# Kernel tuning notes

Hardware: AMD Instinct MI355X
Metric: run time of the kernel (lower is better)

Reference implementation:

```python
import jax
import jax.numpy as jnp
import numpy as np

KSIZE, STRIDE, RATE, FUSE_K, SCALE = 3, 1, 2, 3, 10.0
ESCAPE_NAN = 1e-4


def _same_pad(x, k, s):
    # replicates torch same_padding: asymmetric zero pad so out = ceil(H/s)
    H, W = x.shape[2], x.shape[3]
    oh, ow = -(-H // s), -(-W // s)
    ph = max(0, (oh - 1) * s + k - H)
    pw = max(0, (ow - 1) * s + k - W)
    return jnp.pad(x, ((0, 0), (0, 0), (ph // 2, ph - ph // 2), (pw // 2, pw - pw // 2)))


def _extract_patches(x, k, s):
    # torch extract_image_patches: -> [B, L, C, k, k] with L = out_h*out_w
    x = _same_pad(x, k, s)
    B, C, H, W = x.shape
    Ho, Wo = (H - k) // s + 1, (W - k) // s + 1
    slices = [x[:, :, i:i + Ho * s:s, j:j + Wo * s:s] for i in range(k) for j in range(k)]
    p = jnp.stack(slices, axis=2).reshape(B, C, k, k, Ho, Wo)
    return p.transpose(0, 4, 5, 1, 2, 3).reshape(B, Ho * Wo, C, k, k)


def _contextual_attention(f, b, mask):
    dn = ('NCHW', 'OIHW', 'NCHW')
    # raw background patches for the final deconv: k = 2*rate, stride = rate
    raw_pat = _extract_patches(b, 2 * RATE, RATE * STRIDE)  # [B, L, C, 4, 4]
    # nearest-neighbor 1/rate downsample (torch F.interpolate nearest, sf=0.5)
    f_ds = f[:, :, ::RATE, ::RATE]
    b_ds = b[:, :, ::RATE, ::RATE]
    m_ds = mask[:, :, ::RATE, ::RATE]
    B, C, Hf, Wf = f_ds.shape
    Hb, Wb = b_ds.shape[2], b_ds.shape[3]
    b_pat = _extract_patches(b_ds, KSIZE, STRIDE)  # [B, L, C, 3, 3], L = Hb*Wb
    m_pat = _extract_patches(m_ds, KSIZE, STRIDE)[0]  # [L, 1, 3, 3] (first sample only, as in torch)
    mm = (jnp.mean(m_pat, axis=(1, 2, 3)) == 0.0).astype(f.dtype)[None, :, None, None]  # [1, L, 1, 1]
    fuse_w = jnp.eye(FUSE_K, dtype=f.dtype).reshape(1, 1, FUSE_K, FUSE_K)

    def per_item(xi, wi, raw_wi):
        # xi: [C,Hf,Wf]; wi: [L,C,3,3]; raw_wi: [L,C,4,4]
        max_wi = jnp.sqrt(jnp.sum(wi * wi + ESCAPE_NAN, axis=(1, 2, 3), keepdims=True))
        wi_n = wi / max_wi
        # matching conv: scores [1, L, Hf, Wf]
        yi = jax.lax.conv_general_dilated(xi[None], wi_n, (1, 1), ((1, 1), (1, 1)), dimension_numbers=dn)
        # fuse: identity-diagonal 3x3 conv along (bg_idx, fg_idx) twice with transposes
        yi = yi.reshape(1, 1, Hb * Wb, Hf * Wf)
        yi = jax.lax.conv_general_dilated(yi, fuse_w, (1, 1), ((1, 1), (1, 1)), dimension_numbers=dn)
        yi = yi.reshape(Hb, Wb, Hf, Wf).transpose(1, 0, 3, 2).reshape(1, 1, Hb * Wb, Hf * Wf)
        yi = jax.lax.conv_general_dilated(yi, fuse_w, (1, 1), ((1, 1), (1, 1)), dimension_numbers=dn)
        yi = yi.reshape(Wb, Hb, Wf, Hf).transpose(1, 0, 3, 2).reshape(1, Hb * Wb, Hf, Wf)
        yi = yi * mm
        yi = jax.nn.softmax(yi * SCALE, axis=1) * mm
        # conv_transpose2d(yi, raw_wi[I=L,O=C], stride=rate, padding=1) / 4
        w2 = jnp.flip(raw_wi, (2, 3)).transpose(1, 0, 2, 3)  # [C, L, 4, 4]
        pad = 2 * RATE - 1 - 1  # k - 1 - torch_padding = 2
        out = jax.lax.conv_general_dilated(yi, w2, (1, 1), ((pad, pad), (pad, pad)),
                                           lhs_dilation=(RATE, RATE), dimension_numbers=dn) / 4.0
        return out[0]

    return jax.vmap(per_item)(f_ds, b_pat, raw_pat)  # [B, C, H, W]


def setup_inputs() -> dict:
    key = jax.random.key(0)
    k1, k2 = jax.random.split(key)
    B, C, H, W = 2, 128, 128, 128
    f = jax.random.normal(k1, (B, C, H, W), dtype=jnp.float32)
    b = jax.random.normal(k2, (B, C, H, W), dtype=jnp.float32)
    mask = jnp.zeros((B, 1, H, W), dtype=jnp.float32)
    return {"f": f, "b": b, "mask": mask}


def reference(f, b, mask):
    return _contextual_attention(f, b, mask)
```

## Files before the change

### kernel.cpp

```cpp
#include <hip/hip_runtime.h>
#include <math.h>

#define CDIM 128
#define HF   128
#define WF   128
#define NP   4096
#define NCHUNK 64

typedef __attribute__((ext_vector_type(8))) short short8;
typedef __attribute__((ext_vector_type(16))) float f16a;
typedef float __attribute__((ext_vector_type(4), aligned(16))) f4a16;
typedef float __attribute__((ext_vector_type(4), aligned(4)))  f4u;

__device__ inline ushort f2bf(float x) {
  union { float f; unsigned u; } v; v.f = x;
  unsigned r = v.u + 0x7fff + ((v.u >> 16) & 1);
  return (ushort)(r >> 16);
}
__device__ inline float bf2f(ushort h) {
  union { unsigned u; float f; } v; v.u = ((unsigned)h) << 16; return v.f;
}

__device__ inline void gl2lds16(const ushort* g, ushort* l) {
  __builtin_amdgcn_global_load_lds((const __attribute__((address_space(1))) void*)g,
                                   (__attribute__((address_space(3))) void*)l, 16, 0, 0);
}

__global__ __launch_bounds__(256) void k_prep(const float* __restrict__ f,
                                              const float* __restrict__ b,
                                              ushort* __restrict__ fcat,
                                              ushort* __restrict__ bcat,
                                              float* __restrict__ s2) {
  int idx = blockIdx.x * 256 + threadIdx.x;
  int c = idx & 127, pos = idx >> 7;
  int x = pos & 63, y = pos >> 6;
  int src = c * 16384 + y * 256 + x * 2;
  float fv = f[src], bv = b[src];
  ushort fh = f2bf(fv); ushort fl = f2bf(fv - bf2f(fh));
  ushort bh = f2bf(bv); ushort bl = f2bf(bv - bf2f(bh));
  size_t base = (size_t)pos * 384;
  fcat[base + c] = fh; fcat[base + 128 + c] = fl; fcat[base + 256 + c] = fh;
  bcat[base + c] = bh; bcat[base + 128 + c] = bh; bcat[base + 256 + c] = bl;
  float sq = bv * bv;
#pragma unroll
  for (int off = 32; off; off >>= 1) sq += __shfl_down(sq, off);
  __shared__ float wsum[4];
  if ((threadIdx.x & 63) == 0) wsum[threadIdx.x >> 6] = sq;
  __syncthreads();
  if (threadIdx.x == 0) s2[blockIdx.x * 2]     = wsum[0] + wsum[1];
  if (threadIdx.x == 1) s2[blockIdx.x * 2 + 1] = wsum[2] + wsum[3];
}

__global__ __launch_bounds__(256) void k_mmpnorm(const float* __restrict__ mask,
                                                 const float* __restrict__ s2,
                                                 float* __restrict__ mmp,
                                                 float* __restrict__ rnrm) {
  int bx = blockIdx.x, t = threadIdx.x;
  if (bx < 16) {
    int a = bx * 256 + t;
    int yb = a & 63, xb = a >> 6;
    float s = 0.f;
    for (int dy = -1; dy <= 1; ++dy)
      for (int dx = -1; dx <= 1; ++dx) {
        int y = yb + dy, x = xb + dx;
        if ((unsigned)y < 64u && (unsigned)x < 64u)
          s += mask[y * 256 + x * 2];
      }
    mmp[a] = (s == 0.0f) ? 1.0f : 0.0f;
  } else {
    int p = (bx - 16) * 256 + t;
    int xb = p & 63, yb = p >> 6;
    float s = 0.f;
    for (int dy = -1; dy <= 1; ++dy)
      for (int dx = -1; dx <= 1; ++dx) {
        int y = yb + dy, x = xb + dx;
        if ((unsigned)y < 64u && (unsigned)x < 64u) s += s2[y * 64 + x];
      }
    rnrm[p] = rsqrtf(s + 1152.0f * 1.0e-4f);
  }
}

__global__ __launch_bounds__(512) void k_mfma_gemm(const ushort* __restrict__ A,
                                                   const ushort* __restrict__ B,
                                                   float* __restrict__ Out,
                                                   int Kdim, int lda, int ldb, int ldo,
                                                   long osplit) {
  __shared__ ushort As[2][256 * 64];
  __shared__ ushort Bs[2][256 * 64];
  const int tid = threadIdx.x;
  const int wave = tid >> 6, lane = tid & 63;
  const int l32 = lane & 31, khalf = lane >> 5;

  unsigned nbx = gridDim.x, nby = gridDim.y;
  unsigned lid = blockIdx.x + nbx * (blockIdx.y + nby * blockIdx.z);
  unsigned cpx = (nbx * nby * gridDim.z) >> 3;
  unsigned swz = (lid & 7) * cpx + (lid >> 3);
  unsigned bx = swz % nbx;
  unsigned tmp = swz / nbx;
  unsigned by = tmp % nby, bz = tmp / nby;

  const int m0 = by * 256, n0 = bx * 256;
  const int wm = (wave >> 2) * 128, wn = (wave & 3) * 64;
  const int srow = lane >> 3;
  const int gperm = ((lane & 7) ^ srow) * 8;

  const int koff = bz * Kdim;
  A += koff; B += koff;
  Out += (size_t)bz * osplit;

  const ushort* Ag = A + (size_t)(m0 + wave * 8 + srow) * lda + gperm;
  const ushort* Bg = B + (size_t)(n0 + wave * 8 + srow) * ldb + gperm;
  ushort* AsW = &As[0][0] + (wave * 8) * 64;
  ushort* BsW = &Bs[0][0] + (wave * 8) * 64;

#define STG_A(sl, tt, q) gl2lds16(Ag + (size_t)((q) * 64) * lda + ((tt) << 6), \
                                  AsW + (sl) * 16384 + (q) * 4096)
#define STG_B(sl, tt, q) gl2lds16(Bg + (size_t)((q) * 64) * ldb + ((tt) << 6), \
                                  BsW + (sl) * 16384 + (q) * 4096)

  f16a acc[4][2];
#pragma unroll
  for (int u = 0; u < 4; ++u)
#pragma unroll
    for (int v = 0; v < 2; ++v)
#pragma unroll
      for (int r = 0; r < 16; ++r) acc[u][v][r] = 0.f;

  const int NT = Kdim >> 6;

#pragma unroll
  for (int q = 0; q < 4; ++q) { STG_A(0, 0, q); STG_B(0, 0, q); }
  if (NT > 1) {
#pragma unroll
    for (int q = 0; q < 4; ++q) { STG_A(1, 1, q); STG_B(1, 1, q); }
    asm volatile("s_waitcnt vmcnt(8)" ::: "memory");
  } else {
    asm volatile("s_waitcnt vmcnt(0)" ::: "memory");
  }
  __builtin_amdgcn_s_barrier();

  for (int t = 0; t < NT; ++t) {
    const int sl = t & 1;
    const ushort* Ar = &As[sl][0];
    const ushort* Br = &Bs[sl][0];
    short8 af[2][4], bf[2][2];

#define FRAG_READS(sidx) do { \
  _Pragma("unroll") for (int u = 0; u < 4; ++u) { \
    int am = wm + u * 32 + l32; \
    int ga = (((sidx) * 2 + khalf) ^ (am & 7)) * 8; \
    af[(sidx) & 1][u] = *reinterpret_cast<const short8*>(&Ar[am * 64 + ga]); } \
  _Pragma("unroll") for (int v = 0; v < 2; ++v) { \
    int bn = wn + v * 32 + l32; \
    int gb = (((sidx) * 2 + khalf) ^ (bn & 7)) * 8; \
    bf[(sidx) & 1][v] = *reinterpret_cast<const short8*>(&Br[bn * 64 + gb]); } \
} while (0)

    FRAG_READS(0);
#pragma unroll
    for (int s = 0; s < 4; ++s) {
      if (s == 1) FRAG_READS(2);
      if (s == 2) FRAG_READS(3);
      if (s == 0) FRAG_READS(1);
      if (s == 3) {
        asm volatile("s_waitcnt lgkmcnt(0)" ::: "memory");
        __builtin_amdgcn_sched_barrier(0);
        __builtin_amdgcn_s_barrier();
        __builtin_amdgcn_sched_barrier(0);
        if (t + 2 < NT) {
#pragma unroll
          for (int q = 0; q < 4; ++q) { STG_A(sl, t + 2, q); STG_B(sl, t + 2, q); }
        }
        __builtin_amdgcn_s_setprio(1);
      }
#pragma unroll
      for (int u = 0; u < 4; ++u)
#pragma unroll
        for (int v = 0; v < 2; ++v)
          acc[u][v] = __builtin_amdgcn_mfma_f32_32x32x16_bf16(af[s & 1][u], bf[s & 1][v],
                                                              acc[u][v], 0, 0, 0);
      if (s == 3) __builtin_amdgcn_s_setprio(0);
    }
    if (t + 1 < NT) {
      if (t + 2 < NT) asm volatile("s_waitcnt vmcnt(8)" ::: "memory");
      else            asm volatile("s_waitcnt vmcnt(0)" ::: "memory");
      __builtin_amdgcn_s_barrier();
    }
#undef FRAG_READS
  }

#pragma unroll
  for (int u = 0; u < 4; ++u)
#pragma unroll
    for (int v = 0; v < 2; ++v)
#pragma unroll
      for (int r = 0; r < 16; ++r) {
        int row = (r & 3) + 8 * (r >> 2) + 4 * khalf;
        Out[(size_t)(m0 + wm + u * 32 + row) * ldo + (n0 + wn + v * 32 + l32)] = acc[u][v][r];
      }
#undef STG_A
#undef STG_B
}

__global__ __launch_bounds__(256) void k_s0(const float* __restrict__ D,
                                            const float* __restrict__ rnrm,
                                            float* __restrict__ S0) {
  int p = ((blockIdx.x & 7) << 9) | (blockIdx.x >> 3);
  int yb = p >> 6, xb = p & 63;
  float rp = rnrm[p];
  int t = threadIdx.x;
#pragma unroll
  for (int it = 0; it < 4; ++it) {
    int q = (it * 256 + t) << 2;
    int qy = q >> 6, qx = q & 63;
    f4a16 acc = (f4a16){0.f, 0.f, 0.f, 0.f};
#pragma unroll
    for (int dy = -1; dy <= 1; ++dy) {
      if ((unsigned)(yb + dy) >= 64u) continue;
      if ((unsigned)(qy + dy) >= 64u) continue;
#pragma unroll
      for (int dx = -1; dx <= 1; ++dx) {
        if ((unsigned)(xb + dx) >= 64u) continue;
        int delta = dy * 64 + dx;
        const float* base = D + (size_t)(p + delta) * 4096;
        f4u v;
        if (dx == -1 && qx == 0) {
          f4u r = *(const f4u*)(base + q + delta + 1);
          v = (f4u){0.f, r.x, r.y, r.z};
        } else {
          v = *(const f4u*)(base + q + delta);
          if (dx == 1 && qx == 60) v.w = 0.f;
        }
        acc += v;
      }
    }
    acc *= rp;
    *(f4a16*)(S0 + ((size_t)p << 12) + q) = acc;
  }
}

__global__ __launch_bounds__(256) void k_fuse1(const float* __restrict__ S0,
                                               float* __restrict__ Yp) {
  __shared__ float row[4160];
  int i = ((blockIdx.x & 7) << 9) | (blockIdx.x >> 3);
  int t = threadIdx.x;
  const float* r0 = S0 + (size_t)(i - 1) * 4096;
  const float* r1 = S0 + (size_t)i * 4096;
  const float* r2 = S0 + (size_t)(i + 1) * 4096;
  bool up = (i > 0), dn = (i < 4095);
#pragma unroll
  for (int jj = 0; jj < 4; ++jj) {
    int j = (jj * 256 + t) << 2;
    f4u s = *(const f4u*)(r1 + j);
    if (up) {
      f4u a;
      if (j == 0) { f4u r = *(const f4u*)r0; a = (f4u){0.f, r.x, r.y, r.z}; }
      else a = *(const f4u*)(r0 + j - 1);
      s += a;
    }
    if (dn) {
      f4u d = *(const f4u*)(r2 + j + 1);
      if (j == 4092) d.w = 0.f;
      s += d;
    }
    int base = j + (j >> 6);
    row[base + 0] = s.x; row[base + 1] = s.y; row[base + 2] = s.z; row[base + 3] = s.w;
  }
  __syncthreads();
  int a = ((i & 63) << 6) | (i >> 6);
  float* orow = Yp + ((size_t)a << 12);
#pragma unroll
  for (int bb = 0; bb < 4; ++bb) {
    int b4 = (bb * 256 + t) << 2;
    f4a16 o;
#pragma unroll
    for (int k = 0; k < 4; ++k) {
      int jT = (((b4 + k) & 63) << 6) | ((b4 + k) >> 6);
      o[k] = row[jT + (jT >> 6)];
    }
    *(f4a16*)(orow + b4) = o;
  }
}

__global__ __launch_bounds__(256) void k_smax_part(const float* __restrict__ Yp,
                                                   const float* __restrict__ mmp,
                                                   float* __restrict__ pm,
                                                   float* __restrict__ ps) {
  int v = (blockIdx.x * 256 + threadIdx.x) << 2;
  int chunk = blockIdx.y;
  f4a16 m = (f4a16){-1e30f, -1e30f, -1e30f, -1e30f};
  f4a16 s = (f4a16){0.f, 0.f, 0.f, 0.f};
  int u0 = chunk * (4096 / NCHUNK);
  for (int u = u0; u < u0 + (4096 / NCHUNK); ++u) {
    const float* row = Yp + ((size_t)u << 12);
    f4u tv = *(const f4u*)(row + v);
    if (u > 0) {
      f4u a;
      if (v == 0) { f4u r = *(const f4u*)(row - 4096); a = (f4u){0.f, r.x, r.y, r.z}; }
      else a = *(const f4u*)(row - 4096 + v - 1);
      tv += a;
    }
    if (u < 4095) {
      f4u d = *(const f4u*)(row + 4096 + v + 1);
      if (v == 4092) d.w = 0.f;
      tv += d;
    }
    float g = 10.0f * mmp[u];
    f4u x = tv * g;
#pragma unroll
    for (int l = 0; l < 4; ++l) {
      float xl = x[l];
      if (xl > m[l]) { s[l] = s[l] * __expf(m[l] - xl) + 1.0f; m[l] = xl; }
      else           { s[l] += __expf(xl - m[l]); }
    }
  }
  *(f4a16*)(pm + chunk * NP + v) = m;
  *(f4a16*)(ps + chunk * NP + v) = s;
}

__global__ __launch_bounds__(256) void k_epilogue(const float* __restrict__ Yp,
                                                  const float* __restrict__ pm,
                                                  const float* __restrict__ ps,
                                                  const float* __restrict__ mmp,
                                                  ushort* __restrict__ AT,
                                                  const float* __restrict__ bimg,
                                                  ushort* __restrict__ VtT) {
  __shared__ float T[64][65];
  __shared__ float pmS[4][64];
  __shared__ float psS[4][64];
  __shared__ float mS[64];
  __shared__ float rsS[64];
  int gx = blockIdx.x;
  int t = threadIdx.x;
  if (gx < 4096) {
    int a0 = (gx & 63) * 64, b0 = (gx >> 6) * 64;
    int j = t & 63, grp = t >> 6;
    float m = -1e30f, s = 0.f;
    for (int ch = grp * 16; ch < grp * 16 + 16; ++ch) {
      float m2 = pm[ch * NP + b0 + j], s2 = ps[ch * NP + b0 + j];
      if (m2 > m) { s = s * __expf(m - m2) + s2; m = m2; }
      else        { s += s2 * __expf(m2 - m); }
    }
    pmS[grp][j] = m; psS[grp][j] = s;
    __syncthreads();
    if (grp == 0) {
      for (int g2 = 1; g2 < 4; ++g2) {
        float m2 = pmS[g2][j], s2 = psS[g2][j];
        if (m2 > m) { s = s * __expf(m - m2) + s2; m = m2; }
        else        { s += s2 * __expf(m2 - m); }
      }
      mS[j] = m; rsS[j] = 1.0f / s;
    }
    __syncthreads();
    int i = t >> 4, j4 = (t & 15) << 2;
    f4a16 mc = *(const f4a16*)&mS[j4];
    f4a16 rs = *(const f4a16*)&rsS[j4];
#pragma unroll
    for (int r = 0; r < 4; ++r) {
      int al = r * 16 + i;
      int a = a0 + al;
      const float* row = Yp + ((size_t)a << 12);
      int b = b0 + j4;
      f4u y = *(const f4u*)(row + b);
      if (a > 0) {
        f4u u_;
        if (b == 0) { f4u rr = *(const f4u*)(row - 4096); u_ = (f4u){0.f, rr.x, rr.y, rr.z}; }
        else u_ = *(const f4u*)(row - 4096 + b - 1);
        y += u_;
      }
      if (a < 4095) {
        f4u d = *(const f4u*)(row + 4096 + b + 1);
        if (b == 4092) d.w = 0.f;
        y += d;
      }
      float g = mmp[a];
      f4u x = y * (10.0f * g);
#pragma unroll
      for (int l = 0; l < 4; ++l)
        T[al][j4 + l] = g * __expf(x[l] - mc[l]) * rs[l];
    }
    __syncthreads();
    int by0 = b0 >> 6;
    int cgrp = (t & 7) * 8;
#pragma unroll
    for (int pass = 0; pass < 2; ++pass) {
      int bl = pass * 32 + (t >> 3);
      int q = bl * 64 + by0;
      uint4 w;
      w.x = (unsigned)f2bf(T[cgrp + 0][bl]) | ((unsigned)f2bf(T[cgrp + 1][bl]) << 16);
      w.y = (unsigned)f2bf(T[cgrp + 2][bl]) | ((unsigned)f2bf(T[cgrp + 3][bl]) << 16);
      w.z = (unsigned)f2bf(T[cgrp + 4][bl]) | ((unsigned)f2bf(T[cgrp + 5][bl]) << 16);
      w.w = (unsigned)f2bf(T[cgrp + 6][bl]) | ((unsigned)f2bf(T[cgrp + 7][bl]) << 16);
      *(uint4*)(AT + ((size_t)q << 12) + a0 + cgrp) = w;
    }
  } else {
    int k2 = gx - 4096;
    int c = k2 >> 4, dy = (k2 >> 2) & 3, dx = k2 & 3;
    int px = t & 63;
#pragma unroll
    for (int r = 0; r < 16; ++r) {
      int py = r * 4 + (t >> 6);
      int sy = 2 * py + dy - 1, sx = 2 * px + dx - 1;
      float v = 0.f;
      if ((unsigned)sy < (unsigned)HF && (unsigned)sx < (unsigned)WF)
        v = bimg[c * 16384 + sy * 128 + sx];
      T[py][px] = v;
    }
    __syncthreads();
    ushort* orow = VtT + (size_t)k2 * 4096;
#pragma unroll
    for (int r = 0; r < 16; ++r) {
      int a = r * 256 + t;
      orow[a] = f2bf(T[a & 63][a >> 6]);
    }
  }
}

__global__ __launch_bounds__(256) void k_scatter(const float* __restrict__ Ma,
                                                 const float* __restrict__ Mb,
                                                 float* __restrict__ out) {
  int bid = ((blockIdx.x & 7) << 10) | (blockIdx.x >> 3);
  int idx = bid * 256 + threadIdx.x;
  int ox = idx & 127, oy = (idx >> 7) & 127, c = idx >> 14;
  int qy[2], dyv[2], qx[2], dxv[2];
  if (oy & 1) { qy[0] = (oy - 1) >> 1; dyv[0] = 2; qy[1] = (oy + 1) >> 1; dyv[1] = 0; }
  else        { qy[0] = (oy >> 1) - 1; dyv[0] = 3; qy[1] = oy >> 1;       dyv[1] = 1; }
  if (ox & 1) { qx[0] = (ox - 1) >> 1; dxv[0] = 2; qx[1] = (ox + 1) >> 1; dxv[1] = 0; }
  else        { qx[0] = (ox >> 1) - 1; dxv[0] = 3; qx[1] = ox >> 1;       dxv[1] = 1; }
  float s = 0.f;
#pragma unroll
  for (int i = 0; i < 2; ++i) {
    if ((unsigned)qy[i] >= 64u) continue;
#pragma unroll
    for (int j = 0; j < 2; ++j) {
      if ((unsigned)qx[j] >= 64u) continue;
      int k = c * 16 + dyv[i] * 4 + dxv[j];
      size_t off = (size_t)k * NP + qy[i] * 64 + qx[j];
      s += Ma[off] + Mb[off];
    }
  }
  out[idx] = 0.25f * s;
}

extern "C" void kernel_launch(void* const* d_in, const int* in_sizes, int n_in,
                              void* d_out, int out_size, void* d_ws, size_t ws_size,
                              hipStream_t stream) {
  const float* f_all = (const float*)d_in[0];
  const float* b_all = (const float*)d_in[1];
  const float* m_all = (const float*)d_in[2];
  float* out = (float*)d_out;

  float* ws = (float*)d_ws;
  float* bufD = ws;
  float* bufS = ws + 16777216;
  ushort* fcat = (ushort*)bufS;
  ushort* bcat = (ushort*)(bufS + 786432);
  float* S0  = bufS;
  float* Yp  = bufD;
  ushort* AT  = (ushort*)bufS;
  ushort* VtT = (ushort*)(bufS + 8388608);
  float* M0 = bufD;
  float* M1 = bufD + 8388608;
  float* smalls = ws + 2 * 16777216;
  float* s2    = smalls;
  float* rnrm  = s2 + 4096;
  float* mmp   = rnrm + 4096;
  float* pm    = mmp + 4096;
  float* ps    = pm + NCHUNK * NP;

  const size_t zsF = (size_t)CDIM * HF * WF;
  const size_t zsM = (size_t)HF * WF;

  for (int it = 0; it < 2; ++it) {
    const float* f = f_all + it * zsF;
    const float* b = b_all + it * zsF;
    const float* mk = m_all + it * zsM;
    float* o = out + it * zsF;

    k_prep<<<2048, 256, 0, stream>>>(f, b, fcat, bcat, s2);
    k_mmpnorm<<<32, 256, 0, stream>>>(mk, s2, mmp, rnrm);
    k_mfma_gemm<<<dim3(16, 16, 1), 512, 0, stream>>>(bcat, fcat, bufD, 384, 384, 384, NP, 0);
    k_s0<<<4096, 256, 0, stream>>>(bufD, rnrm, S0);
    k_fuse1<<<4096, 256, 0, stream>>>(S0, Yp);
    k_smax_part<<<dim3(4, NCHUNK), 256, 0, stream>>>(Yp, mmp, pm, ps);
    k_epilogue<<<6144, 256, 0, stream>>>(Yp, pm, ps, mmp, AT, b, VtT);
    k_mfma_gemm<<<dim3(16, 8, 2), 512, 0, stream>>>(VtT, AT, M0, 2048, NP, NP, NP,
                                                    (long)2048 * 4096);
    k_scatter<<<8192, 256, 0, stream>>>(M0, M1, o);
  }
}
```

Measured before the change: 604.5 us.

## Fuse S0 stencil and first fuse pass into one LDS-staged kernel

Merges the 3x3 diagonal stencil kernel (k_s0) and the first fuse/transpose kernel (k_fuse1) into a single kernel. Each block computes 4 output rows plus 2 halo rows of S0 into shared memory, then forms the diagonal fuse sum and the transposed write directly from there. This removes the 64 MB round trip of the S0 intermediate through global memory and one launch. In exchange it recomputes 2 halo rows per 4 rows, about 50% extra stencil work, and uses about 100 KB of LDS per block, which limits occupancy. Workspace buffer roles are reassigned to match.

Measured after the change: 660.2 us. 9.2% more time.

```diff
diff --git a/kernel.cpp b/kernel.cpp
--- a/kernel.cpp
+++ b/kernel.cpp
@@ -202,83 +202,89 @@
 #undef STG_B
 }
 
-__global__ __launch_bounds__(256) void k_s0(const float* __restrict__ D,
-                                            const float* __restrict__ rnrm,
-                                            float* __restrict__ S0) {
-  int p = ((blockIdx.x & 7) << 9) | (blockIdx.x >> 3);
-  int yb = p >> 6, xb = p & 63;
-  float rp = rnrm[p];
-  int t = threadIdx.x;
-#pragma unroll
-  for (int it = 0; it < 4; ++it) {
-    int q = (it * 256 + t) << 2;
-    int qy = q >> 6, qx = q & 63;
-    f4a16 acc = (f4a16){0.f, 0.f, 0.f, 0.f};
-#pragma unroll
-    for (int dy = -1; dy <= 1; ++dy) {
-      if ((unsigned)(yb + dy) >= 64u) continue;
-      if ((unsigned)(qy + dy) >= 64u) continue;
-#pragma unroll
-      for (int dx = -1; dx <= 1; ++dx) {
-        if ((unsigned)(xb + dx) >= 64u) continue;
-        int delta = dy * 64 + dx;
-        const float* base = D + (size_t)(p + delta) * 4096;
-        f4u v;
-        if (dx == -1 && qx == 0) {
-          f4u r = *(const f4u*)(base + q + delta + 1);
-          v = (f4u){0.f, r.x, r.y, r.z};
-        } else {
-          v = *(const f4u*)(base + q + delta);
-          if (dx == 1 && qx == 60) v.w = 0.f;
-        }
-        acc += v;
-      }
-    }
-    acc *= rp;
-    *(f4a16*)(S0 + ((size_t)p << 12) + q) = acc;
-  }
-}
-
-__global__ __launch_bounds__(256) void k_fuse1(const float* __restrict__ S0,
-                                               float* __restrict__ Yp) {
-  __shared__ float row[4160];
-  int i = ((blockIdx.x & 7) << 9) | (blockIdx.x >> 3);
-  int t = threadIdx.x;
-  const float* r0 = S0 + (size_t)(i - 1) * 4096;
-  const float* r1 = S0 + (size_t)i * 4096;
-  const float* r2 = S0 + (size_t)(i + 1) * 4096;
-  bool up = (i > 0), dn = (i < 4095);
-#pragma unroll
-  for (int jj = 0; jj < 4; ++jj) {
-    int j = (jj * 256 + t) << 2;
-    f4u s = *(const f4u*)(r1 + j);
-    if (up) {
-      f4u a;
-      if (j == 0) { f4u r = *(const f4u*)r0; a = (f4u){0.f, r.x, r.y, r.z}; }
-      else a = *(const f4u*)(r0 + j - 1);
-      s += a;
-    }
-    if (dn) {
-      f4u d = *(const f4u*)(r2 + j + 1);
-      if (j == 4092) d.w = 0.f;
-      s += d;
-    }
-    int base = j + (j >> 6);
-    row[base + 0] = s.x; row[base + 1] = s.y; row[base + 2] = s.z; row[base + 3] = s.w;
-  }
+__device__ inline f4a16 s0_tap4(const float* __restrict__ D, int j, int q, float rp) {
+  int yb = j >> 6, xb = j & 63;
+  int qy = q >> 6, qx = q & 63;
+  f4a16 acc = (f4a16){0.f, 0.f, 0.f, 0.f};
+#pragma unroll
+  for (int dy = -1; dy <= 1; ++dy) {
+    if ((unsigned)(yb + dy) >= 64u) continue;
+    if ((unsigned)(qy + dy) >= 64u) continue;
+#pragma unroll
+    for (int dx = -1; dx <= 1; ++dx) {
+      if ((unsigned)(xb + dx) >= 64u) continue;
+      int delta = dy * 64 + dx;
+      const float* base = D + (size_t)(j + delta) * 4096;
+      f4u v;
+      if (dx == -1 && qx == 0) {
+        f4u r = *(const f4u*)(base + q + delta + 1);
+        v = (f4u){0.f, r.x, r.y, r.z};
+      } else {
+        v = *(const f4u*)(base + q + delta);
+        if (dx == 1 && qx == 60) v.w = 0.f;
+      }
+      acc += v;
+    }
+  }
+  return acc * rp;
+}
+
+__global__ __launch_bounds__(512) void k_s0f1(const float* __restrict__ D,
+                                              const float* __restrict__ rnrm,
+                                              float* __restrict__ Yp) {
+  __shared__ float L[6][4162];
+  int bid = blockIdx.x;
+  int swzb = ((bid & 7) << 7) | (bid >> 3);
+  int j0 = swzb * 4;
+  int tid = threadIdx.x;
+
+#pragma unroll
+  for (int r = 0; r < 6; ++r) {
+    int j = j0 - 1 + r;
+    if ((unsigned)j < 4096u) {
+      float rp = rnrm[j];
+#pragma unroll
+      for (int c = 0; c < 2; ++c) {
+        int q = (c * 512 + tid) << 2;
+        f4a16 a = s0_tap4(D, j, q, rp);
+        int ix = 1 + q + (q >> 6);
+        L[r][ix] = a.x; L[r][ix + 1] = a.y; L[r][ix + 2] = a.z; L[r][ix + 3] = a.w;
+      }
+    } else {
+#pragma unroll
+      for (int c = 0; c < 2; ++c) {
+        int q = (c * 512 + tid) << 2;
+        int ix = 1 + q + (q >> 6);
+        L[r][ix] = 0.f; L[r][ix + 1] = 0.f; L[r][ix + 2] = 0.f; L[r][ix + 3] = 0.f;
+      }
+    }
+  }
+  if (tid < 6) { L[tid][0] = 0.f; L[tid][4161] = 0.f; }
   __syncthreads();
-  int a = ((i & 63) << 6) | (i >> 6);
-  float* orow = Yp + ((size_t)a << 12);
-#pragma unroll
-  for (int bb = 0; bb < 4; ++bb) {
-    int b4 = (bb * 256 + t) << 2;
-    f4a16 o;
-#pragma unroll
-    for (int k = 0; k < 4; ++k) {
-      int jT = (((b4 + k) & 63) << 6) | ((b4 + k) >> 6);
-      o[k] = row[jT + (jT >> 6)];
-    }
-    *(f4a16*)(orow + b4) = o;
+
+#pragma unroll
+  for (int g = 0; g < 4; ++g) {
+    int i = j0 + g;
+    int a = ((i & 63) << 6) | (i >> 6);
+    float* orow = Yp + ((size_t)a << 12);
+    const float* Lm = L[g];
+    const float* Lc = L[g + 1];
+    const float* Lp = L[g + 2];
+#pragma unroll
+    for (int bb = 0; bb < 2; ++bb) {
+      int b4 = (bb * 512 + tid) << 2;
+      f4a16 o;
+#pragma unroll
+      for (int k = 0; k < 4; ++k) {
+        int b = b4 + k;
+        int jT = ((b & 63) << 6) | (b >> 6);
+        int ixm = (jT == 0) ? 0 : (jT + ((jT - 1) >> 6));
+        int ixc = 1 + jT + (jT >> 6);
+        int ixp = 2 + jT + ((jT + 1) >> 6);
+        o[k] = Lm[ixm] + Lc[ixc] + Lp[ixp];
+      }
+      *(f4a16*)(orow + b4) = o;
+    }
   }
 }
 
@@ -455,12 +461,12 @@
   float* bufS = ws + 16777216;
   ushort* fcat = (ushort*)bufS;
   ushort* bcat = (ushort*)(bufS + 786432);
-  float* S0  = bufS;
-  float* Yp  = bufD;
-  ushort* AT  = (ushort*)bufS;
-  ushort* VtT = (ushort*)(bufS + 8388608);
-  float* M0 = bufD;
-  float* M1 = bufD + 8388608;
+  float* D   = bufD;
+  float* Yp  = bufS;
+  ushort* AT  = (ushort*)bufD;
+  ushort* VtT = (ushort*)(bufD + 8388608);
+  float* M0 = bufS;
+  float* M1 = bufS + 8388608;
   float* smalls = ws + 2 * 16777216;
   float* s2    = smalls;
   float* rnrm  = s2 + 4096;
@@ -479,9 +485,8 @@
 
     k_prep<<<2048, 256, 0, stream>>>(f, b, fcat, bcat, s2);
     k_mmpnorm<<<32, 256, 0, stream>>>(mk, s2, mmp, rnrm);
-    k_mfma_gemm<<<dim3(16, 16, 1), 512, 0, stream>>>(bcat, fcat, bufD, 384, 384, 384, NP, 0);
-    k_s0<<<4096, 256, 0, stream>>>(bufD, rnrm, S0);
-    k_fuse1<<<4096, 256, 0, stream>>>(S0, Yp);
+    k_mfma_gemm<<<dim3(16, 16, 1), 512, 0, stream>>>(bcat, fcat, D, 384, 384, 384, NP, 0);
+    k_s0f1<<<1024, 512, 0, stream>>>(D, rnrm, Yp);
     k_smax_part<<<dim3(4, NCHUNK), 256, 0, stream>>>(Yp, mmp, pm, ps);
     k_epilogue<<<6144, 256, 0, stream>>>(Yp, pm, ps, mmp, AT, b, VtT);
     k_mfma_gemm<<<dim3(16, 8, 2), 512, 0, stream>>>(VtT, AT, M0, 2048, NP, NP, NP,
```
